# Kernel tuning notes

Measured on AMD Instinct MI355X. Metric: run time of the kernel, lower is better.

The kernel has to match this reference:

```python
import jax, jax.numpy as jnp
import numpy as np

B, S, H = 4, 2048, 1024
E, K = 8, 2

def setup_inputs() -> dict:
    key = jax.random.key(0)
    ks = jax.random.split(key, 5)
    scale = 1.0 / np.sqrt(H)
    return {
        "x": jax.random.normal(ks[0], (B, S, H), dtype=jnp.float32),
        "router_w": jax.random.uniform(ks[1], (E, H), jnp.float32, -scale, scale),
        "router_b": jax.random.uniform(ks[2], (E,), jnp.float32, -scale, scale),
        "expert_w": jax.random.uniform(ks[3], (E, H, H), jnp.float32, -scale, scale),
        "expert_b": jax.random.uniform(ks[4], (E, H), jnp.float32, -scale, scale),
    }


def reference(x, router_w, router_b, expert_w, expert_b):
    # Router: [b,s,E]
    scores = jnp.einsum("bsh,eh->bse", x, router_w) + router_b
    probs = jax.nn.softmax(scores, axis=-1)
    p, expert_id = jax.lax.top_k(probs, K)          # [b,s,K]
    # Renormalize top-k probs (matches p / p.sum(dim=2))
    p = p / jnp.sum(p, axis=-1, keepdims=True)
    # Per-token combine weight per expert: [b,s,E]
    onehot = jax.nn.one_hot(expert_id, E, dtype=x.dtype)  # [b,s,K,E]
    w_comb = jnp.einsum("bske,bsk->bse", onehot, p)
    # All-expert linear (Linear: x @ W.T + b): [b,s,E,h]
    all_out = jnp.einsum("bsh,edh->bsed", x, expert_w) + expert_b
    # Weighted combine over selected experts: [b,s,h]
    return jnp.einsum("bse,bsed->bsd", w_comb, all_out)
```

## Files before the change

kernel.cpp:

```cpp
#include <hip/hip_runtime.h>
#include <hip/hip_bf16.h>
#include <math.h>

#define TOK 8192
#define HD 1024
#define NE 8
#define SLOTS 17408
#define NGRP 512
#define GRPSZ 16

typedef _Float16 half8 __attribute__((ext_vector_type(8)));
typedef _Float16 half4v __attribute__((ext_vector_type(4)));
typedef float floatx4 __attribute__((ext_vector_type(4)));

#define WAIT_VMCNT(N) asm volatile("s_waitcnt vmcnt(" #N ")" ::: "memory")
#define MEMFENCE() asm volatile("" ::: "memory")

__global__ __launch_bounds__(256) void score_cvt(
    const float* __restrict__ x,
    const float* __restrict__ rw,
    const float* __restrict__ rb,
    const float* __restrict__ ew,
    _Float16* __restrict__ xh,
    _Float16* __restrict__ wh,
    int* __restrict__ epair,
    float* __restrict__ w1out,
    int* __restrict__ hist) {
  const int tid = threadIdx.x;
  const int blk = blockIdx.x;
  if (blk >= NGRP) {
    const int g = (blk - NGRP) * 256 + tid;
    const float4* src = (const float4*)ew;
    half4v* dst = (half4v*)wh;
#pragma unroll
    for (int j = 0; j < 4; ++j) {
      float4 v = src[g + 524288 * j];
      half4v h = {(_Float16)v.x, (_Float16)v.y, (_Float16)v.z, (_Float16)v.w};
      dst[g + 524288 * j] = h;
    }
    return;
  }
  const int lane = tid & 63;
  const int wid = tid >> 6;
  __shared__ int hcnt[NE];
  if (tid < NE) hcnt[tid] = 0;
  __syncthreads();

#pragma unroll
  for (int i = 0; i < 4; ++i) {
    const int t = blk * GRPSZ + wid * 4 + i;
    const float4* xp = (const float4*)(x + (size_t)t * HD);
    float4 xr[4];
#pragma unroll
    for (int k = 0; k < 4; ++k) xr[k] = xp[lane + 64 * k];
    _Float16* xo = xh + (size_t)t * HD;
#pragma unroll
    for (int k = 0; k < 4; ++k) {
      half4v h = {(_Float16)xr[k].x, (_Float16)xr[k].y,
                  (_Float16)xr[k].z, (_Float16)xr[k].w};
      *(half4v*)(xo + (lane + 64 * k) * 4) = h;
    }
    float sc[NE];
#pragma unroll
    for (int e = 0; e < NE; ++e) {
      const float4* wp = (const float4*)(rw + e * HD);
      float a = 0.f;
#pragma unroll
      for (int k = 0; k < 4; ++k) {
        float4 w = wp[lane + 64 * k];
        a += xr[k].x * w.x + xr[k].y * w.y + xr[k].z * w.z + xr[k].w * w.w;
      }
#pragma unroll
      for (int off = 32; off > 0; off >>= 1) a += __shfl_xor(a, off);
      sc[e] = a + rb[e];
    }
    float b1 = sc[0]; int e1 = 0;
#pragma unroll
    for (int e = 1; e < NE; ++e) if (sc[e] > b1) { b1 = sc[e]; e1 = e; }
    float b2 = -1e30f; int e2 = 0;
#pragma unroll
    for (int e = 0; e < NE; ++e) { if (e != e1 && sc[e] > b2) { b2 = sc[e]; e2 = e; } }
    if (lane == 0) {
      epair[t] = e1 | (e2 << 8);
      w1out[t] = 1.f / (1.f + expf(b2 - b1));
      atomicAdd(&hcnt[e1], 1);
      atomicAdd(&hcnt[e2], 1);
    }
  }
  __syncthreads();
  if (tid < NE) hist[tid * NGRP + blk] = hcnt[tid];
}

__global__ __launch_bounds__(256) void moe_scatter(
    const int* __restrict__ hist,
    const int* __restrict__ epair,
    const float* __restrict__ w1in,
    int* __restrict__ cntp,
    int* __restrict__ basep,
    int* __restrict__ tok_list,
    float* __restrict__ tok_w,
    int* __restrict__ slot_of) {
  const int tid = threadIdx.x;
  const int blk = blockIdx.x;
  __shared__ int pre_s[NE], tot_s[NE], alloc_s[NE];
  {
    const int e = tid >> 5;
    const int sl = tid & 31;
    int p = 0, tt = 0;
#pragma unroll
    for (int j = 0; j < 16; ++j) {
      int g = sl + 32 * j;
      int h = hist[e * NGRP + g];
      tt += h;
      p += (g < blk) ? h : 0;
    }
#pragma unroll
    for (int off = 16; off > 0; off >>= 1) {
      p += __shfl_xor(p, off);
      tt += __shfl_xor(tt, off);
    }
    if (sl == 0) { pre_s[e] = p; tot_s[e] = tt; }
  }
  __syncthreads();
  if (tid == 0) {
    int b = 0;
    for (int e = 0; e < NE; ++e) {
      alloc_s[e] = b + pre_s[e];
      if (blk == 0) { cntp[e * 64] = tot_s[e]; basep[e] = b; }
      b += (tot_s[e] + 127) & ~127;
    }
  }
  __syncthreads();
  if (tid < GRPSZ) {
    const int t = blk * GRPSZ + tid;
    int ep = epair[t];
    int e1 = ep & 0xff, e2 = ep >> 8;
    float w1 = w1in[t];
    int s1 = atomicAdd(&alloc_s[e1], 1);
    tok_list[s1] = t; tok_w[s1] = w1; slot_of[2 * t] = s1;
    int s2 = atomicAdd(&alloc_s[e2], 1);
    tok_list[s2] = t; tok_w[s2] = 1.f - w1; slot_of[2 * t + 1] = s2;
  }
}

template <int EPI>
__global__ __launch_bounds__(256, 2) void moe_gemm(
    const _Float16* __restrict__ Ah, const _Float16* __restrict__ Bh,
    const float* __restrict__ eb,
    const int* __restrict__ cntp, const int* __restrict__ base,
    const int* __restrict__ tok_list, const float* __restrict__ tok_w,
    _Float16* __restrict__ scratch, float* __restrict__ out) {
  const int e = blockIdx.z;
  const int ce = cntp[e * 64];
  const int mt = ((blockIdx.y >> 3) << 3) | blockIdx.x;
  const int m0 = mt << 7;
  if (m0 >= ce) return;
  const int n0 = (blockIdx.y & 7) << 7;
  const int sbase = base[e];
  const int tid = threadIdx.x;
  const int lane = tid & 63;
  const int wid = tid >> 6;
  const int wm = wid & 1, wn = wid >> 1;

  __shared__ _Float16 A_s[2][128 * 64];
  __shared__ _Float16 B_s[2][128 * 64];
  __shared__ int tok_s[128];
  __shared__ float w_s[128];

  if (tid < 128) {
    int tk = 0; float w = 0.f;
    if (m0 + tid < ce) { tk = tok_list[sbase + m0 + tid]; w = tok_w[sbase + m0 + tid]; }
    tok_s[tid] = tk; w_s[tid] = w;
  }
  __syncthreads();

  floatx4 acc[4][4];
  floatx4 zero = {0.f, 0.f, 0.f, 0.f};
#pragma unroll
  for (int i = 0; i < 4; ++i)
#pragma unroll
    for (int j = 0; j < 4; ++j) acc[i][j] = zero;

  const int wbase = e * HD * HD;
  const int rloc = lane >> 3, sub = lane & 7;
  int agoff[4], bgoff[4];
#pragma unroll
  for (int q = 0; q < 4; ++q) {
    int row = wid * 32 + q * 8 + rloc;
    int g = sub ^ (row & 7);
    agoff[q] = tok_s[row] * HD + g * 8;
    bgoff[q] = wbase + (n0 + row) * HD + g * 8;
  }
  const int l15 = lane & 15, q4 = lane >> 4;

  auto stage = [&](int buf, int k0) {
#pragma unroll
    for (int q = 0; q < 4; ++q) {
      const int r0 = wid * 32 + q * 8;
      __builtin_amdgcn_global_load_lds(
          (const __attribute__((address_space(1))) unsigned int*)(Ah + agoff[q] + k0),
          (__attribute__((address_space(3))) unsigned int*)&A_s[buf][r0 * 64], 16, 0, 0);
      __builtin_amdgcn_global_load_lds(
          (const __attribute__((address_space(1))) unsigned int*)(Bh + bgoff[q] + k0),
          (__attribute__((address_space(3))) unsigned int*)&B_s[buf][r0 * 64], 16, 0, 0);
    }
  };

  auto compute = [&](int buf) {
#pragma unroll
    for (int kf = 0; kf < 2; ++kf) {
      half8 afr[4], bfr[4];
      const int cc = kf * 4 + q4;
#pragma unroll
      for (int i = 0; i < 4; ++i)
        afr[i] = *(const half8*)&A_s[buf][(wm * 64 + i * 16 + l15) * 64 + ((cc ^ (l15 & 7)) * 8)];
#pragma unroll
      for (int j = 0; j < 4; ++j)
        bfr[j] = *(const half8*)&B_s[buf][(wn * 64 + j * 16 + l15) * 64 + ((cc ^ (l15 & 7)) * 8)];
#pragma unroll
      for (int i = 0; i < 4; ++i)
#pragma unroll
        for (int j = 0; j < 4; ++j)
          acc[i][j] = __builtin_amdgcn_mfma_f32_16x16x32_f16(afr[i], bfr[j], acc[i][j], 0, 0, 0);
    }
  };

  stage(0, 0);
  for (int t = 0; t < 15; ++t) {
    stage((t + 1) & 1, (t + 1) * 64);
    WAIT_VMCNT(8);
    __builtin_amdgcn_s_barrier();
    MEMFENCE();
    compute(t & 1);
    MEMFENCE();
    __builtin_amdgcn_s_barrier();
  }
  WAIT_VMCNT(0);
  __builtin_amdgcn_s_barrier();
  MEMFENCE();
  compute(1);

#pragma unroll
  for (int j = 0; j < 4; ++j) {
    int col = n0 + wn * 64 + j * 16 + l15;
    float bias = eb[e * HD + col];
#pragma unroll
    for (int i = 0; i < 4; ++i) {
      int rbase = wm * 64 + i * 16 + (q4 << 2);
#pragma unroll
      for (int r = 0; r < 4; ++r) {
        int row = rbase + r;
        float v = w_s[row] * (acc[i][j][r] + bias);
        if (EPI == 1) {
          scratch[(size_t)(sbase + m0 + row) * HD + col] = (_Float16)v;
        } else {
          if (m0 + row < ce)
            atomicAdd(&out[(size_t)tok_s[row] * HD + col], v);
        }
      }
    }
  }
}

__global__ void moe_combine(const _Float16* __restrict__ scratch,
                            const int* __restrict__ slot_of,
                            float* __restrict__ out) {
  const int tid = threadIdx.x;
  const int t = blockIdx.x * 2 + (tid >> 7);
  const int c = (tid & 127) * 8;
  int sa = slot_of[2 * t], sb = slot_of[2 * t + 1];
  half8 a = *(const half8*)&scratch[(size_t)sa * HD + c];
  half8 b = *(const half8*)&scratch[(size_t)sb * HD + c];
  float* o = out + (size_t)t * HD + c;
  float4 o0 = {(float)a[0] + (float)b[0], (float)a[1] + (float)b[1],
               (float)a[2] + (float)b[2], (float)a[3] + (float)b[3]};
  float4 o1 = {(float)a[4] + (float)b[4], (float)a[5] + (float)b[5],
               (float)a[6] + (float)b[6], (float)a[7] + (float)b[7]};
  *(float4*)o = o0;
  *(float4*)(o + 4) = o1;
}

extern "C" void kernel_launch(void* const* d_in, const int* in_sizes, int n_in,
                              void* d_out, int out_size, void* d_ws, size_t ws_size,
                              hipStream_t stream) {
  (void)in_sizes; (void)n_in;
  const float* x  = (const float*)d_in[0];
  const float* rw = (const float*)d_in[1];
  const float* rb = (const float*)d_in[2];
  const float* ew = (const float*)d_in[3];
  const float* eb = (const float*)d_in[4];
  float* out = (float*)d_out;

  char* w = (char*)d_ws;
  int*   cntp     = (int*)(w + 0);
  int*   basep    = (int*)(w + 2048);
  int*   hist     = (int*)(w + 2304);
  size_t off = 2304 + (size_t)NE * NGRP * 4;
  int*   tok_list = (int*)(w + off);  off += (size_t)SLOTS * 4;
  float* tok_w    = (float*)(w + off); off += (size_t)SLOTS * 4;
  int*   slot_of  = (int*)(w + off);  off += (size_t)TOK * 8;
  int*   epair    = (int*)(w + off);  off += (size_t)TOK * 4;
  float* w1buf    = (float*)(w + off); off += (size_t)TOK * 4;
  off = (off + 255) & ~255ull;
  size_t xh_off = off;
  size_t wh_off = xh_off + (size_t)TOK * HD * 2;
  size_t scr_off = wh_off + (size_t)NE * HD * HD * 2;
  size_t needscr = scr_off + (size_t)SLOTS * HD * 2;
  bool fastscr = ws_size >= needscr;

  if (!fastscr)
    hipMemsetAsync(d_out, 0, (size_t)out_size * sizeof(float), stream);

  _Float16* xh = (_Float16*)(w + xh_off);
  _Float16* wh = (_Float16*)(w + wh_off);
  _Float16* scr = fastscr ? (_Float16*)(w + scr_off) : nullptr;

  score_cvt<<<NGRP + 2048, 256, 0, stream>>>(x, rw, rb, ew, xh, wh,
                                             epair, w1buf, hist);
  moe_scatter<<<NGRP, 256, 0, stream>>>(hist, epair, w1buf, cntp, basep,
                                        tok_list, tok_w, slot_of);

  dim3 grid(HD / 128, TOK / 128, NE);
  if (fastscr) {
    moe_gemm<1><<<grid, 256, 0, stream>>>(xh, wh, eb, cntp, basep,
                                          tok_list, tok_w, scr, out);
    moe_combine<<<TOK / 2, 256, 0, stream>>>(scr, slot_of, out);
  } else {
    moe_gemm<0><<<grid, 256, 0, stream>>>(xh, wh, eb, cntp, basep,
                                          tok_list, tok_w, nullptr, out);
  }
}
```

Measured before the change: 195.1 us.

## Enlarge MoE GEMM tile to 256x256 with 8 waves and interleaved LDS pipeline

The grouped expert GEMM now uses 256x256 output tiles computed by 512 threads (8 waves, each owning 128x64), where it previously used 128x128 tiles with 256 threads. Per-expert slot padding grows to multiples of 256 to match. The K loop splits into four MFMA quadrants, with A and B next-tile loads issued between them, s_setprio raised around the MFMA bursts, and sched_barriers added. The grid is reordered so the expert index is fastest-varying. Larger tiles halve global and LDS traffic per FLOP, but padding waste grows, fewer blocks are launched, and the 128 KB of LDS may limit occupancy to one block per CU.

```diff
diff --git a/kernel.cpp b/kernel.cpp
--- a/kernel.cpp
+++ b/kernel.cpp
@@ -5,7 +5,7 @@
 #define TOK 8192
 #define HD 1024
 #define NE 8
-#define SLOTS 17408
+#define SLOTS 18432
 #define NGRP 512
 #define GRPSZ 16
 
@@ -13,8 +13,8 @@
 typedef _Float16 half4v __attribute__((ext_vector_type(4)));
 typedef float floatx4 __attribute__((ext_vector_type(4)));
 
-#define WAIT_VMCNT(N) asm volatile("s_waitcnt vmcnt(" #N ")" ::: "memory")
-#define MEMFENCE() asm volatile("" ::: "memory")
+#define WAIT_VMCNT0() asm volatile("s_waitcnt vmcnt(0)" ::: "memory")
+#define WAIT_LGKM0()  asm volatile("s_waitcnt lgkmcnt(0)" ::: "memory")
 
 __global__ __launch_bounds__(256) void score_cvt(
     const float* __restrict__ x,
@@ -127,7 +127,7 @@
     for (int e = 0; e < NE; ++e) {
       alloc_s[e] = b + pre_s[e];
       if (blk == 0) { cntp[e * 64] = tot_s[e]; basep[e] = b; }
-      b += (tot_s[e] + 127) & ~127;
+      b += (tot_s[e] + 255) & ~255;
     }
   }
   __syncthreads();
@@ -144,113 +144,176 @@
 }
 
 template <int EPI>
-__global__ __launch_bounds__(256, 2) void moe_gemm(
+__global__ __launch_bounds__(512, 2) void moe_gemm(
     const _Float16* __restrict__ Ah, const _Float16* __restrict__ Bh,
     const float* __restrict__ eb,
     const int* __restrict__ cntp, const int* __restrict__ base,
     const int* __restrict__ tok_list, const float* __restrict__ tok_w,
     _Float16* __restrict__ scratch, float* __restrict__ out) {
-  const int e = blockIdx.z;
+  const int e = blockIdx.x;
   const int ce = cntp[e * 64];
-  const int mt = ((blockIdx.y >> 3) << 3) | blockIdx.x;
-  const int m0 = mt << 7;
+  const int m0 = (blockIdx.y >> 2) << 8;
   if (m0 >= ce) return;
-  const int n0 = (blockIdx.y & 7) << 7;
+  const int nb = (blockIdx.y & 3) << 8;
   const int sbase = base[e];
   const int tid = threadIdx.x;
   const int lane = tid & 63;
   const int wid = tid >> 6;
-  const int wm = wid & 1, wn = wid >> 1;
-
-  __shared__ _Float16 A_s[2][128 * 64];
-  __shared__ _Float16 B_s[2][128 * 64];
-  __shared__ int tok_s[128];
-  __shared__ float w_s[128];
-
-  if (tid < 128) {
+  const int wm = wid >> 2, wn = wid & 3;
+
+  __shared__ _Float16 A_s[2][256 * 64];
+  __shared__ _Float16 B_s[2][256 * 64];
+  __shared__ int tok_s[256];
+  __shared__ float w_s[256];
+
+  if (tid < 256) {
     int tk = 0; float w = 0.f;
     if (m0 + tid < ce) { tk = tok_list[sbase + m0 + tid]; w = tok_w[sbase + m0 + tid]; }
     tok_s[tid] = tk; w_s[tid] = w;
   }
   __syncthreads();
 
-  floatx4 acc[4][4];
+  floatx4 acc[8][4];
   floatx4 zero = {0.f, 0.f, 0.f, 0.f};
 #pragma unroll
-  for (int i = 0; i < 4; ++i)
+  for (int i = 0; i < 8; ++i)
 #pragma unroll
     for (int j = 0; j < 4; ++j) acc[i][j] = zero;
 
   const int wbase = e * HD * HD;
   const int rloc = lane >> 3, sub = lane & 7;
+  const int g8 = (sub ^ rloc) * 8;
   int agoff[4], bgoff[4];
 #pragma unroll
-  for (int q = 0; q < 4; ++q) {
-    int row = wid * 32 + q * 8 + rloc;
-    int g = sub ^ (row & 7);
-    agoff[q] = tok_s[row] * HD + g * 8;
-    bgoff[q] = wbase + (n0 + row) * HD + g * 8;
+  for (int u = 0; u < 4; ++u) {
+    const int row = u * 64 + wid * 8 + rloc;
+    agoff[u] = tok_s[row] * HD + g8;
+    bgoff[u] = wbase + (nb + row) * HD + g8;
   }
   const int l15 = lane & 15, q4 = lane >> 4;
-
-  auto stage = [&](int buf, int k0) {
-#pragma unroll
-    for (int q = 0; q < 4; ++q) {
-      const int r0 = wid * 32 + q * 8;
+  const int ck0 = ((q4)     ^ (l15 & 7)) * 8;
+  const int ck1 = ((4 + q4) ^ (l15 & 7)) * 8;
+  const int arow0 = (wm * 128 + l15) * 64;
+  const int brow0 = (wn * 64  + l15) * 64;
+
+  auto stageA = [&](int buf, int k0) {
+#pragma unroll
+    for (int u = 0; u < 4; ++u) {
+      const int r0 = u * 64 + wid * 8;
       __builtin_amdgcn_global_load_lds(
-          (const __attribute__((address_space(1))) unsigned int*)(Ah + agoff[q] + k0),
+          (const __attribute__((address_space(1))) unsigned int*)(Ah + agoff[u] + k0),
           (__attribute__((address_space(3))) unsigned int*)&A_s[buf][r0 * 64], 16, 0, 0);
+    }
+  };
+  auto stageB = [&](int buf, int k0) {
+#pragma unroll
+    for (int u = 0; u < 4; ++u) {
+      const int r0 = u * 64 + wid * 8;
       __builtin_amdgcn_global_load_lds(
-          (const __attribute__((address_space(1))) unsigned int*)(Bh + bgoff[q] + k0),
+          (const __attribute__((address_space(1))) unsigned int*)(Bh + bgoff[u] + k0),
           (__attribute__((address_space(3))) unsigned int*)&B_s[buf][r0 * 64], 16, 0, 0);
     }
   };
 
-  auto compute = [&](int buf) {
-#pragma unroll
-    for (int kf = 0; kf < 2; ++kf) {
-      half8 afr[4], bfr[4];
-      const int cc = kf * 4 + q4;
-#pragma unroll
-      for (int i = 0; i < 4; ++i)
-        afr[i] = *(const half8*)&A_s[buf][(wm * 64 + i * 16 + l15) * 64 + ((cc ^ (l15 & 7)) * 8)];
-#pragma unroll
-      for (int j = 0; j < 4; ++j)
-        bfr[j] = *(const half8*)&B_s[buf][(wn * 64 + j * 16 + l15) * 64 + ((cc ^ (l15 & 7)) * 8)];
-#pragma unroll
-      for (int i = 0; i < 4; ++i)
-#pragma unroll
-        for (int j = 0; j < 4; ++j)
-          acc[i][j] = __builtin_amdgcn_mfma_f32_16x16x32_f16(afr[i], bfr[j], acc[i][j], 0, 0, 0);
-    }
-  };
-
-  stage(0, 0);
-  for (int t = 0; t < 15; ++t) {
-    stage((t + 1) & 1, (t + 1) * 64);
-    WAIT_VMCNT(8);
-    __builtin_amdgcn_s_barrier();
-    MEMFENCE();
-    compute(t & 1);
-    MEMFENCE();
-    __builtin_amdgcn_s_barrier();
-  }
-  WAIT_VMCNT(0);
+  stageA(0, 0);
+  stageB(0, 0);
+  WAIT_VMCNT0();
   __builtin_amdgcn_s_barrier();
-  MEMFENCE();
-  compute(1);
+
+#pragma unroll 2
+  for (int t = 0; t < 16; ++t) {
+    const int cur = t & 1, nxt = cur ^ 1;
+    const int kn = (t + 1) * 64;
+    half8 afr[4][2], b01[2][2], b23[2][2];
+
+#pragma unroll
+    for (int i = 0; i < 4; ++i) {
+      afr[i][0] = *(const half8*)&A_s[cur][arow0 + i * 16 * 64 + ck0];
+      afr[i][1] = *(const half8*)&A_s[cur][arow0 + i * 16 * 64 + ck1];
+    }
+#pragma unroll
+    for (int j = 0; j < 2; ++j) {
+      b01[j][0] = *(const half8*)&B_s[cur][brow0 + j * 16 * 64 + ck0];
+      b01[j][1] = *(const half8*)&B_s[cur][brow0 + j * 16 * 64 + ck1];
+    }
+    if (t < 15) stageA(nxt, kn);
+    __builtin_amdgcn_s_barrier();
+    WAIT_LGKM0();
+    __builtin_amdgcn_sched_barrier(0);
+    __builtin_amdgcn_s_setprio(1);
+#pragma unroll
+    for (int i = 0; i < 4; ++i)
+#pragma unroll
+      for (int j = 0; j < 2; ++j) {
+        acc[i][j] = __builtin_amdgcn_mfma_f32_16x16x32_f16(afr[i][0], b01[j][0], acc[i][j], 0, 0, 0);
+        acc[i][j] = __builtin_amdgcn_mfma_f32_16x16x32_f16(afr[i][1], b01[j][1], acc[i][j], 0, 0, 0);
+      }
+    __builtin_amdgcn_s_setprio(0);
+    __builtin_amdgcn_s_barrier();
+
+#pragma unroll
+    for (int j = 0; j < 2; ++j) {
+      b23[j][0] = *(const half8*)&B_s[cur][brow0 + (j + 2) * 16 * 64 + ck0];
+      b23[j][1] = *(const half8*)&B_s[cur][brow0 + (j + 2) * 16 * 64 + ck1];
+    }
+    if (t < 15) stageB(nxt, kn);
+    __builtin_amdgcn_s_barrier();
+    WAIT_LGKM0();
+    __builtin_amdgcn_sched_barrier(0);
+    __builtin_amdgcn_s_setprio(1);
+#pragma unroll
+    for (int i = 0; i < 4; ++i)
+#pragma unroll
+      for (int j = 0; j < 2; ++j) {
+        acc[i][j + 2] = __builtin_amdgcn_mfma_f32_16x16x32_f16(afr[i][0], b23[j][0], acc[i][j + 2], 0, 0, 0);
+        acc[i][j + 2] = __builtin_amdgcn_mfma_f32_16x16x32_f16(afr[i][1], b23[j][1], acc[i][j + 2], 0, 0, 0);
+      }
+    __builtin_amdgcn_s_setprio(0);
+    __builtin_amdgcn_s_barrier();
+
+#pragma unroll
+    for (int i = 0; i < 4; ++i) {
+      afr[i][0] = *(const half8*)&A_s[cur][arow0 + (i + 4) * 16 * 64 + ck0];
+      afr[i][1] = *(const half8*)&A_s[cur][arow0 + (i + 4) * 16 * 64 + ck1];
+    }
+    __builtin_amdgcn_s_barrier();
+    WAIT_LGKM0();
+    __builtin_amdgcn_sched_barrier(0);
+    __builtin_amdgcn_s_setprio(1);
+#pragma unroll
+    for (int i = 0; i < 4; ++i)
+#pragma unroll
+      for (int j = 0; j < 2; ++j) {
+        acc[i + 4][j + 2] = __builtin_amdgcn_mfma_f32_16x16x32_f16(afr[i][0], b23[j][0], acc[i + 4][j + 2], 0, 0, 0);
+        acc[i + 4][j + 2] = __builtin_amdgcn_mfma_f32_16x16x32_f16(afr[i][1], b23[j][1], acc[i + 4][j + 2], 0, 0, 0);
+      }
+    __builtin_amdgcn_s_setprio(0);
+    __builtin_amdgcn_s_barrier();
+
+    __builtin_amdgcn_s_setprio(1);
+#pragma unroll
+    for (int i = 0; i < 4; ++i)
+#pragma unroll
+      for (int j = 0; j < 2; ++j) {
+        acc[i + 4][j] = __builtin_amdgcn_mfma_f32_16x16x32_f16(afr[i][0], b01[j][0], acc[i + 4][j], 0, 0, 0);
+        acc[i + 4][j] = __builtin_amdgcn_mfma_f32_16x16x32_f16(afr[i][1], b01[j][1], acc[i + 4][j], 0, 0, 0);
+      }
+    __builtin_amdgcn_s_setprio(0);
+    WAIT_VMCNT0();
+    __builtin_amdgcn_s_barrier();
+  }
 
 #pragma unroll
   for (int j = 0; j < 4; ++j) {
-    int col = n0 + wn * 64 + j * 16 + l15;
-    float bias = eb[e * HD + col];
-#pragma unroll
-    for (int i = 0; i < 4; ++i) {
-      int rbase = wm * 64 + i * 16 + (q4 << 2);
+    const int col = nb + wn * 64 + j * 16 + l15;
+    const float bias = eb[e * HD + col];
+#pragma unroll
+    for (int i = 0; i < 8; ++i) {
+      const int rbase = wm * 128 + i * 16 + (q4 << 2);
 #pragma unroll
       for (int r = 0; r < 4; ++r) {
-        int row = rbase + r;
-        float v = w_s[row] * (acc[i][j][r] + bias);
+        const int row = rbase + r;
+        const float v = w_s[row] * (acc[i][j][r] + bias);
         if (EPI == 1) {
           scratch[(size_t)(sbase + m0 + row) * HD + col] = (_Float16)v;
         } else {
@@ -320,13 +383,13 @@
   moe_scatter<<<NGRP, 256, 0, stream>>>(hist, epair, w1buf, cntp, basep,
                                         tok_list, tok_w, slot_of);
 
-  dim3 grid(HD / 128, TOK / 128, NE);
+  dim3 grid(NE, 256, 1);
   if (fastscr) {
-    moe_gemm<1><<<grid, 256, 0, stream>>>(xh, wh, eb, cntp, basep,
+    moe_gemm<1><<<grid, 512, 0, stream>>>(xh, wh, eb, cntp, basep,
                                           tok_list, tok_w, scr, out);
     moe_combine<<<TOK / 2, 256, 0, stream>>>(scr, slot_of, out);
   } else {
-    moe_gemm<0><<<grid, 256, 0, stream>>>(xh, wh, eb, cntp, basep,
+    moe_gemm<0><<<grid, 512, 0, stream>>>(xh, wh, eb, cntp, basep,
                                           tok_list, tok_w, nullptr, out);
   }
 }
```

Measured after the change: 210.4 us. +7.8%, slower.
